# Kernel optimization log

Hardware: AMD Instinct MI355X
Metric: run time of the kernel (lower is better)

The kernel has to match this reference:

```python
import jax, jax.numpy as jnp
import numpy as np

D = 8  # sheaf block size


def setup_inputs() -> dict:
    key = jax.random.key(0)
    k1, k2, k3 = jax.random.split(key, 3)
    n, e = 1024, 32768
    x = jax.random.normal(k1, (n, D), dtype=jnp.float32)
    edge_index = jax.random.randint(k2, (2, e), 0, n, dtype=jnp.int64)
    # Phi: PyG MLP(num_layers=1, bias=False) == Linear(D, D*D, bias=False), weight [out, in]
    W = jax.random.normal(k3, (D * D, D), dtype=jnp.float32) * (1.0 / np.sqrt(D))
    return {"x": x, "edge_index": edge_index, "W": W}


def reference(x, edge_index, W):
    src, dst = edge_index[0], edge_index[1]
    # sym=True branch: |x_i - x_j| per edge  -> [e, D]
    x_in = jnp.abs(x[src] - x[dst])
    # single linear layer, no bias -> [e, D*D] -> [e, D, D]
    R_tmp = (x_in @ W.T).reshape(-1, D, D)
    n = x.shape[0]
    # dense n x n x D x D output; torch uses empty + indexed assign, we use zeros + scatter-set
    R = jnp.zeros((n, n, D, D), dtype=x.dtype).at[src, dst].set(R_tmp)
    return R
```

## Files before the change

### kernel.cpp

```cpp
#include <hip/hip_runtime.h>

#define D 8

__global__ void sheaf_claim_kernel(const int* __restrict__ src,
                                   const int* __restrict__ dst,
                                   int* __restrict__ out_i, int n, int e) {
    int k = blockIdx.x * blockDim.x + threadIdx.x;
    if (k >= e) return;
    long long pair = (long long)src[k] * (long long)n + (long long)dst[k];
    atomicMax(&out_i[pair * 64], k + 1);
}

__global__ void sheaf_scatter_kernel(const float* __restrict__ x,
                                     const int* __restrict__ src,
                                     const int* __restrict__ dst,
                                     const float* __restrict__ W,
                                     float* __restrict__ out, int n, int e) {
    int gid = blockIdx.x * blockDim.x + threadIdx.x;
    int k = gid >> 6;
    int o = gid & 63;
    if (k >= e) return;

    int s = src[k];
    int d = dst[k];
    long long base = ((long long)s * (long long)n + (long long)d) * 64;

    int claim = __float_as_int(out[base]);
    if (claim != k + 1) return;

    const float* xs = x + s * D;
    const float* xd = x + d * D;
    const float* w  = W + o * D;

    float acc = 0.0f;
#pragma unroll
    for (int i = 0; i < D; ++i) {
        acc += fabsf(xs[i] - xd[i]) * w[i];
    }
    out[base + o] = acc;
}

extern "C" void kernel_launch(void* const* d_in, const int* in_sizes, int n_in,
                              void* d_out, int out_size, void* d_ws, size_t ws_size,
                              hipStream_t stream) {
    const float* x   = (const float*)d_in[0];
    const int*   ei  = (const int*)d_in[1];
    const float* W   = (const float*)d_in[2];

    int n = in_sizes[0] / D;
    int e = in_sizes[1] / 2;
    const int* src = ei;
    const int* dst = ei + e;

    float* out = (float*)d_out;

    hipMemsetAsync(out, 0, (size_t)out_size * sizeof(float), stream);

    {
        int threads = 256;
        int blocks = (e + threads - 1) / threads;
        sheaf_claim_kernel<<<blocks, threads, 0, stream>>>(src, dst, (int*)out, n, e);
    }

    {
        int threads = 256;
        long long total = (long long)e * 64;
        int blocks = (int)((total + threads - 1) / threads);
        sheaf_scatter_kernel<<<blocks, threads, 0, stream>>>(x, src, dst, W, out, n, e);
    }
}
```

Baseline: 266.4 us.

## Claim edges in compact workspace and fuse zero-fill with dense output write

Moves the last-writer claim table from the strided output into a compact per-pair int workspace. A single fused kernel then writes every 8x8 tile exactly once, either zeros or the computed block, with float4 stores. This removes the separate full-output memset and the scattered writes that came after it, so the 256MB output is written once instead of twice. It needs a workspace of n*n ints, and falls back to a plain zero kernel plus scatter path when the workspace is too small.

```diff
diff --git a/kernel.cpp b/kernel.cpp
--- a/kernel.cpp
+++ b/kernel.cpp
@@ -2,70 +2,145 @@
 
 #define D 8
 
-__global__ void sheaf_claim_kernel(const int* __restrict__ src,
-                                   const int* __restrict__ dst,
-                                   int* __restrict__ out_i, int n, int e) {
+
+__global__ void zero_ws_kernel(int* __restrict__ ws, int ntiles) {
+    int i = blockIdx.x * blockDim.x + threadIdx.x;
+    if (i < ntiles) ws[i] = 0;
+}
+
+__global__ void claim_ws_kernel(const int* __restrict__ src,
+                                const int* __restrict__ dst,
+                                int* __restrict__ ws, int n, int e) {
     int k = blockIdx.x * blockDim.x + threadIdx.x;
     if (k >= e) return;
-    long long pair = (long long)src[k] * (long long)n + (long long)dst[k];
+    atomicMax(&ws[src[k] * n + dst[k]], k + 1);
+}
+
+__global__ void fused_out_kernel(const float* __restrict__ x,
+                                 const int* __restrict__ src,
+                                 const int* __restrict__ dst,
+                                 const float* __restrict__ W,
+                                 const int* __restrict__ ws,
+                                 float4* __restrict__ out4,
+                                 int ntiles) {
+    int gid = blockIdx.x * blockDim.x + threadIdx.x;
+    int tile = gid >> 4;
+    int t = gid & 15;
+    if (tile >= ntiles) return;
+
+    int claim = ws[tile];
+    if (claim == 0) {
+        out4[gid] = make_float4(0.f, 0.f, 0.f, 0.f);
+        return;
+    }
+    int k = claim - 1;
+    int s = src[k], d = dst[k];
+    const float* xs = x + s * D;
+    const float* xd = x + d * D;
+
+    float diff[D];
+#pragma unroll
+    for (int i = 0; i < D; ++i) diff[i] = fabsf(xs[i] - xd[i]);
+
+    float4 r;
+    float acc[4];
+#pragma unroll
+    for (int j = 0; j < 4; ++j) {
+        int o = t * 4 + j;
+        const float* w = W + o * D;
+        float a = 0.f;
+#pragma unroll
+        for (int i = 0; i < D; ++i) a += diff[i] * w[i];
+        acc[j] = a;
+    }
+    r.x = acc[0]; r.y = acc[1]; r.z = acc[2]; r.w = acc[3];
+    out4[gid] = r;
+}
+
+
+__global__ void zero_out_kernel(float4* __restrict__ out4, int n4) {
+    int i = blockIdx.x * blockDim.x + threadIdx.x;
+    if (i < n4) out4[i] = make_float4(0.f, 0.f, 0.f, 0.f);
+}
+
+__global__ void claim_out_kernel(const int* __restrict__ src,
+                                 const int* __restrict__ dst,
+                                 int* __restrict__ out_i, int n, int e) {
+    int k = blockIdx.x * blockDim.x + threadIdx.x;
+    if (k >= e) return;
+    long long pair = (long long)src[k] * n + dst[k];
     atomicMax(&out_i[pair * 64], k + 1);
 }
 
-__global__ void sheaf_scatter_kernel(const float* __restrict__ x,
-                                     const int* __restrict__ src,
-                                     const int* __restrict__ dst,
-                                     const float* __restrict__ W,
-                                     float* __restrict__ out, int n, int e) {
+__global__ void scatter_out_kernel(const float* __restrict__ x,
+                                   const int* __restrict__ src,
+                                   const int* __restrict__ dst,
+                                   const float* __restrict__ W,
+                                   float* __restrict__ out, int n, int e) {
     int gid = blockIdx.x * blockDim.x + threadIdx.x;
     int k = gid >> 6;
     int o = gid & 63;
     if (k >= e) return;
-
-    int s = src[k];
-    int d = dst[k];
-    long long base = ((long long)s * (long long)n + (long long)d) * 64;
-
+    int s = src[k], d = dst[k];
+    long long base = ((long long)s * n + d) * 64;
     int claim = __float_as_int(out[base]);
     if (claim != k + 1) return;
-
     const float* xs = x + s * D;
     const float* xd = x + d * D;
-    const float* w  = W + o * D;
-
-    float acc = 0.0f;
+    const float* w = W + o * D;
+    float a = 0.f;
 #pragma unroll
-    for (int i = 0; i < D; ++i) {
-        acc += fabsf(xs[i] - xd[i]) * w[i];
-    }
-    out[base + o] = acc;
+    for (int i = 0; i < D; ++i) a += fabsf(xs[i] - xd[i]) * w[i];
+    out[base + o] = a;
 }
 
 extern "C" void kernel_launch(void* const* d_in, const int* in_sizes, int n_in,
                               void* d_out, int out_size, void* d_ws, size_t ws_size,
                               hipStream_t stream) {
-    const float* x   = (const float*)d_in[0];
-    const int*   ei  = (const int*)d_in[1];
-    const float* W   = (const float*)d_in[2];
+    const float* x  = (const float*)d_in[0];
+    const int*   ei = (const int*)d_in[1];
+    const float* W  = (const float*)d_in[2];
 
     int n = in_sizes[0] / D;
     int e = in_sizes[1] / 2;
     const int* src = ei;
     const int* dst = ei + e;
 
-    float* out = (float*)d_out;
+    int ntiles = out_size / 64;
+    int n4 = out_size / 4;
 
-    hipMemsetAsync(out, 0, (size_t)out_size * sizeof(float), stream);
-
-    {
-        int threads = 256;
-        int blocks = (e + threads - 1) / threads;
-        sheaf_claim_kernel<<<blocks, threads, 0, stream>>>(src, dst, (int*)out, n, e);
-    }
-
-    {
-        int threads = 256;
-        long long total = (long long)e * 64;
-        int blocks = (int)((total + threads - 1) / threads);
-        sheaf_scatter_kernel<<<blocks, threads, 0, stream>>>(x, src, dst, W, out, n, e);
+    if (ws_size >= (size_t)ntiles * sizeof(int)) {
+        int* ws = (int*)d_ws;
+        {
+            int threads = 256, blocks = (ntiles + threads - 1) / threads;
+            zero_ws_kernel<<<blocks, threads, 0, stream>>>(ws, ntiles);
+        }
+        {
+            int threads = 256, blocks = (e + threads - 1) / threads;
+            claim_ws_kernel<<<blocks, threads, 0, stream>>>(src, dst, ws, n, e);
+        }
+        {
+            int threads = 256;
+            long long total = (long long)ntiles * 16;
+            int blocks = (int)((total + threads - 1) / threads);
+            fused_out_kernel<<<blocks, threads, 0, stream>>>(
+                x, src, dst, W, ws, (float4*)d_out, ntiles);
+        }
+    } else {
+        {
+            int threads = 256, blocks = (n4 + threads - 1) / threads;
+            zero_out_kernel<<<blocks, threads, 0, stream>>>((float4*)d_out, n4);
+        }
+        {
+            int threads = 256, blocks = (e + threads - 1) / threads;
+            claim_out_kernel<<<blocks, threads, 0, stream>>>(src, dst, (int*)d_out, n, e);
+        }
+        {
+            int threads = 256;
+            long long total = (long long)e * 64;
+            int blocks = (int)((total + threads - 1) / threads);
+            scatter_out_kernel<<<blocks, threads, 0, stream>>>(
+                x, src, dst, W, (float*)d_out, n, e);
+        }
     }
 }
```

Result: faster. 259.7 us (-2.5%).
